# Optimization experiments

Measured on AMD Instinct MI355X. Metric: run time of the kernel, lower is better.

Reference implementation:

```python
import jax, jax.numpy as jnp
import numpy as np
import math

V, BLOCK, D, L, H, B, T = 32000, 1024, 1024, 6, 16, 4, 1024
HD = D // H
FF = 4 * D


def setup_inputs() -> dict:
    key = jax.random.key(0)
    ks = jax.random.split(key, 16)
    s = 0.02
    inp = {
        "idx": jax.random.randint(ks[0], (B, T), 0, V),
        "tok_emb": s * jax.random.normal(ks[1], (V, D), jnp.float32),
        "pos_emb": jnp.zeros((1, BLOCK, D), jnp.float32) + s * jax.random.normal(ks[2], (1, BLOCK, D), jnp.float32),
        "ln1_g": jnp.ones((L, D), jnp.float32),
        "ln1_b": jnp.zeros((L, D), jnp.float32),
        "qkv_w": s * jax.random.normal(ks[3], (L, 3 * D, D), jnp.float32),
        "proj_w": s * jax.random.normal(ks[4], (L, D, D), jnp.float32),
        "ln2_g": jnp.ones((L, D), jnp.float32),
        "ln2_b": jnp.zeros((L, D), jnp.float32),
        "mlp_w1": s * jax.random.normal(ks[5], (L, FF, D), jnp.float32),
        "mlp_b1": jnp.zeros((L, FF), jnp.float32),
        "mlp_w2": s * jax.random.normal(ks[6], (L, D, FF), jnp.float32),
        "mlp_b2": jnp.zeros((L, D), jnp.float32),
        "lnf_g": jnp.ones((D,), jnp.float32),
        "lnf_b": jnp.zeros((D,), jnp.float32),
        "head_w": s * jax.random.normal(ks[7], (V, D), jnp.float32),
    }
    return inp


def _layernorm(x, g, b, eps=1e-5):
    mu = jnp.mean(x, axis=-1, keepdims=True)
    var = jnp.mean(jnp.square(x - mu), axis=-1, keepdims=True)
    return (x - mu) * jax.lax.rsqrt(var + eps) * g + b


def _attn(x, qkv_w, proj_w):
    b, t, c = x.shape
    qkv = jnp.einsum('btc,fc->btf', x, qkv_w)  # [B,T,3D]
    q, k, v = jnp.split(qkv, 3, axis=-1)
    q = q.reshape(b, t, H, HD)
    k = k.reshape(b, t, H, HD)
    v = v.reshape(b, t, H, HD)
    att = jnp.einsum('bqhd,bkhd->bhqk', q, k) / math.sqrt(HD)
    causal = jnp.tril(jnp.ones((t, t), bool))
    att = jnp.where(causal[None, None], att, -jnp.inf)
    att = jax.nn.softmax(att, axis=-1)
    y = jnp.einsum('bhqk,bkhd->bqhd', att, v).reshape(b, t, c)
    return jnp.einsum('btc,fc->btf', y, proj_w)


def reference(idx, tok_emb, pos_emb, ln1_g, ln1_b, qkv_w, proj_w,
              ln2_g, ln2_b, mlp_w1, mlp_b1, mlp_w2, mlp_b2,
              lnf_g, lnf_b, head_w):
    t = idx.shape[1]
    x = tok_emb[idx] + pos_emb[:, :t, :]
    for i in range(L):
        h = _layernorm(x, ln1_g[i], ln1_b[i])
        x = x + _attn(h, qkv_w[i], proj_w[i])
        h = _layernorm(x, ln2_g[i], ln2_b[i])
        h = jax.nn.gelu(jnp.einsum('btc,fc->btf', h, mlp_w1[i]) + mlp_b1[i], approximate=False)
        x = x + jnp.einsum('btf,cf->btc', h, mlp_w2[i]) + mlp_b2[i]
    x = _layernorm(x, lnf_g, lnf_b)
    logits = jnp.einsum('btc,vc->btv', x, head_w)
    return logits
```

## Files before the change

kernel.cpp:

```cpp
#include <hip/hip_runtime.h>
#include <hip/hip_bf16.h>
#include <math.h>

#define BB 4
#define TT 1024
#define DD 1024
#define HH 16
#define HDIM 64
#define FFD 4096
#define VV 32000
#define LL 6
#define BT (BB * TT)

typedef __bf16 bf16;
typedef bf16 bf16x8 __attribute__((ext_vector_type(8)));
typedef bf16 bf16x4 __attribute__((ext_vector_type(4)));
typedef float f32x4 __attribute__((ext_vector_type(4)));

__device__ __forceinline__ void gload16(const void* g, void* l) {
    __builtin_amdgcn_global_load_lds((__attribute__((address_space(1))) unsigned int*)(g),
                                     (__attribute__((address_space(3))) unsigned int*)(l),
                                     16, 0, 0);
}

__global__ __launch_bounds__(256) void embed_k(const int* __restrict__ idx,
                                               const float* __restrict__ tok,
                                               const float* __restrict__ pos,
                                               float* __restrict__ x) {
    int row = blockIdx.x;
    int tid = threadIdx.x;
    int t = row & (TT - 1);
    int token = idx[row];
    float4 a = *(const float4*)(tok + (size_t)token * DD + tid * 4);
    float4 p = *(const float4*)(pos + (size_t)t * DD + tid * 4);
    *(float4*)(x + (size_t)row * DD + tid * 4) =
        make_float4(a.x + p.x, a.y + p.y, a.z + p.z, a.w + p.w);
}

__global__ __launch_bounds__(256) void cvt_bf16_k(const float* __restrict__ in,
                                                  bf16* __restrict__ out, long n) {
    long i0 = ((long)blockIdx.x * 256 + threadIdx.x) * 8;
    long stride = (long)gridDim.x * 256 * 8;
    for (long i = i0; i < n; i += stride) {
        float4 v0 = *(const float4*)(in + i);
        float4 v1 = *(const float4*)(in + i + 4);
        bf16x8 o;
        o[0] = (bf16)v0.x; o[1] = (bf16)v0.y; o[2] = (bf16)v0.z; o[3] = (bf16)v0.w;
        o[4] = (bf16)v1.x; o[5] = (bf16)v1.y; o[6] = (bf16)v1.z; o[7] = (bf16)v1.w;
        *(bf16x8*)(out + i) = o;
    }
}

__global__ __launch_bounds__(256) void layernorm_k(const float* __restrict__ in,
                                                   bf16* __restrict__ out,
                                                   const float* __restrict__ g,
                                                   const float* __restrict__ b) {
    __shared__ float red[256];
    int row = blockIdx.x;
    int tid = threadIdx.x;
    const float* ip = in + (size_t)row * DD;
    float4 v = *(const float4*)(ip + tid * 4);

    float s = v.x + v.y + v.z + v.w;
    red[tid] = s; __syncthreads();
    for (int st = 128; st > 0; st >>= 1) { if (tid < st) red[tid] += red[tid + st]; __syncthreads(); }
    float mu = red[0] * (1.0f / DD);
    __syncthreads();

    float d0 = v.x - mu, d1 = v.y - mu, d2 = v.z - mu, d3 = v.w - mu;
    red[tid] = d0 * d0 + d1 * d1 + d2 * d2 + d3 * d3; __syncthreads();
    for (int st = 128; st > 0; st >>= 1) { if (tid < st) red[tid] += red[tid + st]; __syncthreads(); }
    float var = red[0] * (1.0f / DD);
    float rs = rsqrtf(var + 1e-5f);

    float4 gv = *(const float4*)(g + tid * 4);
    float4 bv = *(const float4*)(b + tid * 4);
    bf16x4 o;
    o[0] = (bf16)(d0 * rs * gv.x + bv.x);
    o[1] = (bf16)(d1 * rs * gv.y + bv.y);
    o[2] = (bf16)(d2 * rs * gv.z + bv.z);
    o[3] = (bf16)(d3 * rs * gv.w + bv.w);
    *(bf16x4*)(out + (size_t)row * DD + tid * 4) = o;
}

template <bool BIAS, bool GELU, bool OBF>
__global__ __launch_bounds__(512, 2) void gemm_256(const bf16* __restrict__ A,
                                                   const bf16* __restrict__ W,
                                                   const float* __restrict__ bias,
                                                   void* __restrict__ Cv,
                                                   int M, int N, int K) {
    __shared__ char lds[2 * 65536];
    const int tid = threadIdx.x;
    const int lane = tid & 63, wave = tid >> 6;
    const int c = lane & 15, g = lane >> 4;

    const int nm = M >> 8;
    const int nwg = gridDim.x;
    const int wgid = (blockIdx.x & 7) * (nwg >> 3) + (blockIdx.x >> 3);
    const int m0 = (wgid % nm) * 256, n0 = (wgid / nm) * 256;
    const int wm = wave >> 2, wn = wave & 3;

    const int srow = tid >> 2;
    const int lq = (tid & 3) ^ ((tid >> 3) & 3);
    const bf16* Asrc = A + (size_t)(m0 + srow) * K + lq * 8;
    const bf16* Bsrc = W + (size_t)(n0 + srow) * K + lq * 8;
    const size_t K128 = (size_t)128 * K;

    const int key = (c >> 1) & 3;
    const int rdA = (wm * 128 + c) * 64 + ((g ^ key) * 16);
    const int rdB = 32768 + (wn * 64 + c) * 64 + ((g ^ key) * 16);

    f32x4 acc[8][4] = {};
    const int NT = K >> 6;
    const int NH = 4 * NT;

#define STAGEH(H)                                                             \
    if ((H) < NH) {                                                           \
        const int t2_ = (H) >> 2, h_ = (H) & 3;                               \
        const bf16* s_ = ((h_ & 1) ? Bsrc : Asrc) + (size_t)t2_ * 64 + (h_ >> 1) * 32; \
        char* d_ = lds + (t2_ & 1) * 65536 + (h_ & 1) * 32768 + (h_ >> 1) * 16384 + tid * 16; \
        gload16(s_, d_);                                                      \
        gload16(s_ + K128, d_ + 8192);                                        \
    }

#define MFMA16(base)                                                          \
    __builtin_amdgcn_s_setprio(1);                                            \
    _Pragma("unroll")                                                         \
    for (int fi = 0; fi < 4; ++fi) {                                          \
        _Pragma("unroll")                                                     \
        for (int fj = 0; fj < 4; ++fj)                                        \
            acc[(base) + fi][fj] = __builtin_amdgcn_mfma_f32_16x16x32_bf16(   \
                bA[fi], bB[fj], acc[(base) + fi][fj], 0, 0, 0);               \
    }                                                                         \
    __builtin_amdgcn_s_setprio(0);

    STAGEH(0); STAGEH(1); STAGEH(2); STAGEH(3); STAGEH(4);
    asm volatile("s_waitcnt vmcnt(6)" ::: "memory");
    __builtin_amdgcn_sched_barrier(0);
    __builtin_amdgcn_s_barrier();
    __builtin_amdgcn_sched_barrier(0);

    for (int kt = 0; kt < NT; ++kt) {
        const char* bp = lds + (kt & 1) * 65536;
        bf16x8 bA[4], bB[4];
#pragma unroll
        for (int fj = 0; fj < 4; ++fj) bB[fj] = *(const bf16x8*)(bp + rdB + fj * 1024);
#pragma unroll
        for (int fi = 0; fi < 4; ++fi) bA[fi] = *(const bf16x8*)(bp + rdA + fi * 1024);
        STAGEH(4 * kt + 5);
        asm volatile("s_waitcnt lgkmcnt(0)" ::: "memory");
        __builtin_amdgcn_sched_barrier(0);
        MFMA16(0)
#pragma unroll
        for (int fi = 0; fi < 4; ++fi) bA[fi] = *(const bf16x8*)(bp + rdA + (4 + fi) * 1024);
        STAGEH(4 * kt + 6);
        asm volatile("s_waitcnt lgkmcnt(0)" ::: "memory");
        __builtin_amdgcn_sched_barrier(0);
        MFMA16(4)
        if (kt + 1 < NT) { asm volatile("s_waitcnt vmcnt(6)" ::: "memory"); }
        else             { asm volatile("s_waitcnt vmcnt(0)" ::: "memory"); }
        __builtin_amdgcn_sched_barrier(0);
        __builtin_amdgcn_s_barrier();
        __builtin_amdgcn_sched_barrier(0);
#pragma unroll
        for (int fj = 0; fj < 4; ++fj) bB[fj] = *(const bf16x8*)(bp + rdB + 16384 + fj * 1024);
#pragma unroll
        for (int fi = 0; fi < 4; ++fi) bA[fi] = *(const bf16x8*)(bp + rdA + 16384 + fi * 1024);
        STAGEH(4 * kt + 7);
        asm volatile("s_waitcnt lgkmcnt(0)" ::: "memory");
        __builtin_amdgcn_sched_barrier(0);
        MFMA16(0)
#pragma unroll
        for (int fi = 0; fi < 4; ++fi) bA[fi] = *(const bf16x8*)(bp + rdA + 16384 + (4 + fi) * 1024);
        STAGEH(4 * kt + 8);
        asm volatile("s_waitcnt lgkmcnt(0)" ::: "memory");
        __builtin_amdgcn_sched_barrier(0);
        MFMA16(4)
        if (kt + 2 < NT)      { asm volatile("s_waitcnt vmcnt(6)" ::: "memory"); }
        else if (kt + 2 == NT){ asm volatile("s_waitcnt vmcnt(4)" ::: "memory"); }
        __builtin_amdgcn_sched_barrier(0);
        __builtin_amdgcn_s_barrier();
        __builtin_amdgcn_sched_barrier(0);
    }
#undef STAGEH
#undef MFMA16

    const int orow  = m0 + wm * 128 + g * 4;
    const int ocol0 = n0 + wn * 64 + c;
#pragma unroll
    for (int fj = 0; fj < 4; ++fj) {
        const int col = ocol0 + fj * 16;
        float bs = 0.f;
        if (BIAS) bs = bias[col];
#pragma unroll
        for (int fi = 0; fi < 8; ++fi) {
#pragma unroll
            for (int r = 0; r < 4; ++r) {
                int row = orow + fi * 16 + r;
                float v = acc[fi][fj][r] + bs;
                if (GELU) v = 0.5f * v * (1.0f + erff(v * 0.70710678118654752f));
                if (OBF) ((bf16*)Cv)[(size_t)row * N + col] = (bf16)v;
                else     __builtin_nontemporal_store(v, (float*)Cv + (size_t)row * N + col);
            }
        }
    }
}

template <bool ADD, bool BIAS>
__global__ __launch_bounds__(256, 2) void gemm_128p(const bf16* __restrict__ A,
                                                    const bf16* __restrict__ W,
                                                    const float* __restrict__ bias,
                                                    float* __restrict__ C,
                                                    int M, int N, int K) {
    __shared__ char lds[2 * 32768];
    const int tid = threadIdx.x;
    const int lane = tid & 63, wave = tid >> 6;
    const int c = lane & 15, g = lane >> 4;

    const int nm = M >> 7;
    const int nwg = gridDim.x;
    const int wgid = (blockIdx.x & 7) * (nwg >> 3) + (blockIdx.x >> 3);
    const int m0 = (wgid % nm) * 128, n0 = (wgid / nm) * 128;
    const int wm = wave >> 1, wn = wave & 1;

    const int srow = tid >> 2;
    const int lq = (tid & 3) ^ ((tid >> 3) & 3);
    const bf16* Asrc = A + (size_t)(m0 + srow) * K + lq * 8;
    const bf16* Bsrc = W + (size_t)(n0 + srow) * K + lq * 8;
    const size_t K64 = (size_t)64 * K;

    const int key = (c >> 1) & 3;
    const int rdA = (wm * 64 + c) * 64 + ((g ^ key) * 16);
    const int rdB = 16384 + (wn * 64 + c) * 64 + ((g ^ key) * 16);

    f32x4 acc[4][4] = {};
    const int NT = K >> 6;
    const int NH = 4 * NT;

#define STAGEH(H)                                                             \
    if ((H) < NH) {                                                           \
        const int t2_ = (H) >> 2, h_ = (H) & 3;                               \
        const bf16* s_ = ((h_ & 1) ? Bsrc : Asrc) + (size_t)t2_ * 64 + (h_ >> 1) * 32; \
        char* d_ = lds + (t2_ & 1) * 32768 + (h_ & 1) * 16384 + (h_ >> 1) * 8192 + tid * 16; \
        gload16(s_, d_);                                                      \
        gload16(s_ + K64, d_ + 4096);                                         \
    }

#define MFMA16()                                                              \
    __builtin_amdgcn_s_setprio(1);                                            \
    _Pragma("unroll")                                                         \
    for (int fi = 0; fi < 4; ++fi) {                                          \
        _Pragma("unroll")                                                     \
        for (int fj = 0; fj < 4; ++fj)                                       \
            acc[fi][fj] = __builtin_amdgcn_mfma_f32_16x16x32_bf16(            \
                bA[fi], bB[fj], acc[fi][fj], 0, 0, 0);                        \
    }                                                                         \
    __builtin_amdgcn_s_setprio(0);

    STAGEH(0); STAGEH(1); STAGEH(2); STAGEH(3); STAGEH(4); STAGEH(5);
    asm volatile("s_waitcnt vmcnt(8)" ::: "memory");
    __builtin_amdgcn_sched_barrier(0);
    __builtin_amdgcn_s_barrier();
    __builtin_amdgcn_sched_barrier(0);

    for (int kt = 0; kt < NT; ++kt) {
        const char* bp = lds + (kt & 1) * 32768;
        bf16x8 bA[4], bB[4];
#pragma unroll
        for (int fj = 0; fj < 4; ++fj) bB[fj] = *(const bf16x8*)(bp + rdB + fj * 1024);
#pragma unroll
        for (int fi = 0; fi < 4; ++fi) bA[fi] = *(const bf16x8*)(bp + rdA + fi * 1024);
        STAGEH(4 * kt + 6); STAGEH(4 * kt + 7);
        asm volatile("s_waitcnt lgkmcnt(0)" ::: "memory");
        __builtin_amdgcn_sched_barrier(0);
        MFMA16()
        if (kt + 1 < NT) { asm volatile("s_waitcnt vmcnt(8)" ::: "memory"); }
        else             { asm volatile("s_waitcnt vmcnt(0)" ::: "memory"); }
        __builtin_amdgcn_sched_barrier(0);
        __builtin_amdgcn_s_barrier();
        __builtin_amdgcn_sched_barrier(0);
#pragma unroll
        for (int fj = 0; fj < 4; ++fj) bB[fj] = *(const bf16x8*)(bp + rdB + 8192 + fj * 1024);
#pragma unroll
        for (int fi = 0; fi < 4; ++fi) bA[fi] = *(const bf16x8*)(bp + rdA + 8192 + fi * 1024);
        STAGEH(4 * kt + 8); STAGEH(4 * kt + 9);
        asm volatile("s_waitcnt lgkmcnt(0)" ::: "memory");
        __builtin_amdgcn_sched_barrier(0);
        MFMA16()
        if (kt + 2 < NT)       { asm volatile("s_waitcnt vmcnt(8)" ::: "memory"); }
        else if (kt + 2 == NT) { asm volatile("s_waitcnt vmcnt(4)" ::: "memory"); }
        __builtin_amdgcn_sched_barrier(0);
        __builtin_amdgcn_s_barrier();
        __builtin_amdgcn_sched_barrier(0);
    }
#undef STAGEH
#undef MFMA16

    const int orow  = m0 + wm * 64 + g * 4;
    const int ocol0 = n0 + wn * 64 + c;
#pragma unroll
    for (int fj = 0; fj < 4; ++fj) {
        const int col = ocol0 + fj * 16;
        float bs = 0.f;
        if (BIAS) bs = bias[col];
#pragma unroll
        for (int fi = 0; fi < 4; ++fi) {
#pragma unroll
            for (int r = 0; r < 4; ++r) {
                int row = orow + fi * 16 + r;
                float v = acc[fi][fj][r] + bs;
                float* p = C + (size_t)row * N + col;
                if (ADD) *p += v;
                else     __builtin_nontemporal_store(v, p);
            }
        }
    }
}

__global__ __launch_bounds__(256) void vprep_k(const bf16* __restrict__ qkv,
                                               bf16* __restrict__ Vt) {
    __shared__ bf16 Vls[64 * 72];
    const int tid = threadIdx.x;
    const int t0 = blockIdx.x * 64;
    const int h = blockIdx.y, b = blockIdx.z;
    const int row = tid >> 3, ch = tid & 7;

    const bf16* src = qkv + ((size_t)(b * TT + t0 + row)) * 3072 + 2048 + h * 64 + ch * 8;
    bf16x8 v0 = *(const bf16x8*)(src);
    bf16x8 v1 = *(const bf16x8*)(src + (size_t)32 * 3072);
#pragma unroll
    for (int j = 0; j < 8; ++j) {
        Vls[(ch * 8 + j) * 72 + row]      = v0[j];
        Vls[(ch * 8 + j) * 72 + row + 32] = v1[j];
    }
    __syncthreads();

    const int dr = tid >> 3;
    bf16* dst = Vt + ((size_t)((b * HH + h) * 64 + dr)) * 1024 + t0 + ch * 8;
    bf16x8 o0 = *(const bf16x8*)(Vls + dr * 72 + ch * 8);
    bf16x8 o1 = *(const bf16x8*)(Vls + (dr + 32) * 72 + ch * 8);
    *(bf16x8*)(dst) = o0;
    *(bf16x8*)(dst + (size_t)32 * 1024) = o1;
}

__global__ __launch_bounds__(512) void fattn_k(const bf16* __restrict__ qkv,
                                               const bf16* __restrict__ Vt,
                                               bf16* __restrict__ y) {
    __shared__ bf16 Ks[2][64 * 64];
    __shared__ bf16 Vs[2][64 * 64];
    __shared__ bf16 Ps[8][16 * 72];
    const int tid = threadIdx.x, lane = tid & 63, wave = tid >> 6;
    const int g = lane >> 4, c = lane & 15;
    const int q0 = (gridDim.x - 1 - blockIdx.x) * 128;
    const int h = blockIdx.y, b = blockIdx.z;
    const size_t qbase = (size_t)b * TT * 3072;

    const int qrow = q0 + wave * 16 + c;
    const bf16* qp = qkv + qbase + (size_t)qrow * 3072 + h * 64;
    bf16x8 qf0 = *(const bf16x8*)(qp + g * 8);
    bf16x8 qf1 = *(const bf16x8*)(qp + 32 + g * 8);

    const int srow = tid >> 3;
    const int lq = (tid & 7) ^ (srow & 7);
    const bf16* Ksrc = qkv + qbase + 1024 + h * 64 + (size_t)srow * 3072 + lq * 8;
    const bf16* Vsrc = Vt + ((size_t)(b * HH + h) * 64 + srow) * 1024 + lq * 8;

    float mO[4] = {-1e30f, -1e30f, -1e30f, -1e30f};
    float lO[4] = {0.f, 0.f, 0.f, 0.f};
    f32x4 acc[4] = {};

    bf16* pw = Ps[wave];
    const int ntiles = (q0 >> 6) + 2;
    const int qg0 = q0 + wave * 16 + 4 * g;
    const int cs = c & 7;

#define STAGE_KV(t_, buf_)                                                        \
    {                                                                             \
        const int kk_ = (t_) * 64;                                                \
        gload16(Ksrc + (size_t)kk_ * 3072, (char*)Ks[buf_] + tid * 16);           \
        gload16(Vsrc + kk_,                (char*)Vs[buf_] + tid * 16);           \
    }

    STAGE_KV(0, 0)

    for (int t = 0; t < ntiles; ++t) {
        const int k0 = t * 64;
        if (t + 1 < ntiles) {
            STAGE_KV(t + 1, (t + 1) & 1)
            asm volatile("s_waitcnt vmcnt(2)" ::: "memory");
        } else {
            asm volatile("s_waitcnt vmcnt(0)" ::: "memory");
        }
        __builtin_amdgcn_sched_barrier(0);
        __builtin_amdgcn_s_barrier();
        __builtin_amdgcn_sched_barrier(0);

        const bf16* kb = Ks[t & 1];
        const bf16* vb = Vs[t & 1];

        f32x4 s[4] = {};
#pragma unroll
        for (int j = 0; j < 4; ++j) {
            const bf16* kr = kb + (16 * j + c) * 64;
            bf16x8 kf0 = *(const bf16x8*)(kr + ((g ^ cs) * 8));
            bf16x8 kf1 = *(const bf16x8*)(kr + (((4 + g) ^ cs) * 8));
            s[j] = __builtin_amdgcn_mfma_f32_16x16x32_bf16(qf0, kf0, s[j], 0, 0, 0);
            s[j] = __builtin_amdgcn_mfma_f32_16x16x32_bf16(qf1, kf1, s[j], 0, 0, 0);
        }

        float mt_[4];
        bool need = false;
#pragma unroll
        for (int r = 0; r < 4; ++r) {
            const int qg = qg0 + r;
            float a0 = s[0][r] * 0.125f, a1 = s[1][r] * 0.125f;
            float a2 = s[2][r] * 0.125f, a3 = s[3][r] * 0.125f;
            if (k0 + c > qg)      a0 = -1e30f;
            if (k0 + 16 + c > qg) a1 = -1e30f;
            if (k0 + 32 + c > qg) a2 = -1e30f;
            if (k0 + 48 + c > qg) a3 = -1e30f;
            s[0][r] = a0; s[1][r] = a1; s[2][r] = a2; s[3][r] = a3;
            float mt = fmaxf(fmaxf(a0, a1), fmaxf(a2, a3));
            mt = fmaxf(mt, __shfl_xor(mt, 1));
            mt = fmaxf(mt, __shfl_xor(mt, 2));
            mt = fmaxf(mt, __shfl_xor(mt, 4));
            mt = fmaxf(mt, __shfl_xor(mt, 8));
            mt_[r] = mt;
            need |= (mt > mO[r]);
        }
        if (__any(need)) {
#pragma unroll
            for (int r = 0; r < 4; ++r) {
                float mn = fmaxf(mO[r], mt_[r]);
                float sc = __expf(mO[r] - mn);
                mO[r] = mn;
                lO[r] *= sc;
                acc[0][r] *= sc; acc[1][r] *= sc; acc[2][r] *= sc; acc[3][r] *= sc;
            }
        }
#pragma unroll
        for (int r = 0; r < 4; ++r) {
            float e0 = __expf(s[0][r] - mO[r]);
            float e1 = __expf(s[1][r] - mO[r]);
            float e2 = __expf(s[2][r] - mO[r]);
            float e3 = __expf(s[3][r] - mO[r]);
            lO[r] += (e0 + e1) + (e2 + e3);
            bf16* pr = pw + (4 * g + r) * 72;
            pr[c] = (bf16)e0; pr[16 + c] = (bf16)e1;
            pr[32 + c] = (bf16)e2; pr[48 + c] = (bf16)e3;
        }

#pragma unroll
        for (int ks = 0; ks < 2; ++ks) {
            bf16x8 pf = *(const bf16x8*)(pw + c * 72 + ks * 32 + g * 8);
#pragma unroll
            for (int jb = 0; jb < 4; ++jb) {
                const int d = 16 * jb + c;
                bf16x8 vf = *(const bf16x8*)(vb + d * 64 + (((ks * 4 + g) ^ cs) * 8));
                acc[jb] = __builtin_amdgcn_mfma_f32_16x16x32_bf16(pf, vf, acc[jb], 0, 0, 0);
            }
        }
        __builtin_amdgcn_s_barrier();
        __builtin_amdgcn_sched_barrier(0);
    }
#undef STAGE_KV

#pragma unroll
    for (int r = 0; r < 4; ++r) {
        float l = lO[r];
        l += __shfl_xor(l, 1);
        l += __shfl_xor(l, 2);
        l += __shfl_xor(l, 4);
        l += __shfl_xor(l, 8);
        float invl = 1.0f / l;
        size_t orow = (size_t)(b * TT + qg0 + r) * DD + h * 64;
#pragma unroll
        for (int jb = 0; jb < 4; ++jb)
            y[orow + jb * 16 + c] = (bf16)(acc[jb][r] * invl);
    }
}

extern "C" void kernel_launch(void* const* d_in, const int* in_sizes, int n_in,
                              void* d_out, int out_size, void* d_ws, size_t ws_size,
                              hipStream_t stream) {
    const int*   idx     = (const int*)d_in[0];
    const float* tok_emb = (const float*)d_in[1];
    const float* pos_emb = (const float*)d_in[2];
    const float* ln1_g   = (const float*)d_in[3];
    const float* ln1_b   = (const float*)d_in[4];
    const float* qkv_w   = (const float*)d_in[5];
    const float* proj_w  = (const float*)d_in[6];
    const float* ln2_g   = (const float*)d_in[7];
    const float* ln2_b   = (const float*)d_in[8];
    const float* mlp_w1  = (const float*)d_in[9];
    const float* mlp_b1  = (const float*)d_in[10];
    const float* mlp_w2  = (const float*)d_in[11];
    const float* mlp_b2  = (const float*)d_in[12];
    const float* lnf_g   = (const float*)d_in[13];
    const float* lnf_b   = (const float*)d_in[14];
    const float* head_w  = (const float*)d_in[15];
    float* out = (float*)d_out;

    char* ws = (char*)d_ws;
    float* x      = (float*)ws;
    bf16*  qkv_bf = (bf16*)(ws + (16ull << 20));
    bf16*  Vt     = (bf16*)(ws + (40ull << 20));
    bf16*  h_bf   = (bf16*)(ws + (48ull << 20));
    bf16*  y_bf   = (bf16*)(ws + (56ull << 20));
    bf16*  ff_bf  = (bf16*)(ws + (64ull << 20));
    bf16*  wbuf   = (bf16*)(ws + (96ull << 20));
    bf16*  hw_bf  = (bf16*)(ws + (56ull << 20));

    embed_k<<<BT, 256, 0, stream>>>(idx, tok_emb, pos_emb, x);

    for (int l = 0; l < LL; ++l) {
        layernorm_k<<<BT, 256, 0, stream>>>(x, h_bf, ln1_g + (size_t)l * DD, ln1_b + (size_t)l * DD);
        cvt_bf16_k<<<2048, 256, 0, stream>>>(qkv_w + (size_t)l * 3 * DD * DD, wbuf, (long)3 * DD * DD);
        gemm_256<false, false, true><<<(BT / 256) * (3 * DD / 256), 512, 0, stream>>>(
            h_bf, wbuf, nullptr, qkv_bf, BT, 3 * DD, DD);
        vprep_k<<<dim3(TT / 64, HH, BB), 256, 0, stream>>>(qkv_bf, Vt);
        fattn_k<<<dim3(TT / 128, HH, BB), 512, 0, stream>>>(qkv_bf, Vt, y_bf);
        cvt_bf16_k<<<2048, 256, 0, stream>>>(proj_w + (size_t)l * DD * DD, wbuf, (long)DD * DD);
        gemm_128p<true, false><<<(BT / 128) * (DD / 128), 256, 0, stream>>>(
            y_bf, wbuf, nullptr, x, BT, DD, DD);
        layernorm_k<<<BT, 256, 0, stream>>>(x, h_bf, ln2_g + (size_t)l * DD, ln2_b + (size_t)l * DD);
        cvt_bf16_k<<<2048, 256, 0, stream>>>(mlp_w1 + (size_t)l * FFD * DD, wbuf, (long)FFD * DD);
        gemm_256<true, true, true><<<(BT / 256) * (FFD / 256), 512, 0, stream>>>(
            h_bf, wbuf, mlp_b1 + (size_t)l * FFD, ff_bf, BT, FFD, DD);
        cvt_bf16_k<<<2048, 256, 0, stream>>>(mlp_w2 + (size_t)l * DD * FFD, wbuf, (long)DD * FFD);
        gemm_128p<true, true><<<(BT / 128) * (DD / 128), 256, 0, stream>>>(
            ff_bf, wbuf, mlp_b2 + (size_t)l * DD, x, BT, DD, FFD);
    }

    layernorm_k<<<BT, 256, 0, stream>>>(x, h_bf, lnf_g, lnf_b);
    cvt_bf16_k<<<4096, 256, 0, stream>>>(head_w, hw_bf, (long)VV * DD);
    gemm_256<false, false, false><<<(BT / 256) * (VV / 256), 512, 0, stream>>>(
        h_bf, hw_bf, nullptr, out, BT, VV, DD);
}
```

Before: 1.932 ms.

## Use exp2 softmax, skip masking on full tiles, pack P stores with permuted V layout

```diff
diff --git a/kernel.cpp b/kernel.cpp
--- a/kernel.cpp
+++ b/kernel.cpp
@@ -337,8 +337,13 @@
 
     const int dr = tid >> 3;
     bf16* dst = Vt + ((size_t)((b * HH + h) * 64 + dr)) * 1024 + t0 + ch * 8;
-    bf16x8 o0 = *(const bf16x8*)(Vls + dr * 72 + ch * 8);
-    bf16x8 o1 = *(const bf16x8*)(Vls + (dr + 32) * 72 + ch * 8);
+    bf16x8 o0, o1;
+#pragma unroll
+    for (int i = 0; i < 8; ++i) {
+        const int tt = 2 * ch + (i >> 2) + 16 * (i & 3);
+        o0[i] = Vls[dr * 72 + tt];
+        o1[i] = Vls[(dr + 32) * 72 + tt];
+    }
     *(bf16x8*)(dst) = o0;
     *(bf16x8*)(dst + (size_t)32 * 1024) = o1;
 }
@@ -354,6 +359,7 @@
     const int q0 = (gridDim.x - 1 - blockIdx.x) * 128;
     const int h = blockIdx.y, b = blockIdx.z;
     const size_t qbase = (size_t)b * TT * 3072;
+    const float SC = 0.125f * 1.4426950408889634f;
 
     const int qrow = q0 + wave * 16 + c;
     const bf16* qp = qkv + qbase + (size_t)qrow * 3072 + h * 64;
@@ -408,17 +414,20 @@
             s[j] = __builtin_amdgcn_mfma_f32_16x16x32_bf16(qf1, kf1, s[j], 0, 0, 0);
         }
 
+        const bool full = (t + 2 < ntiles);
         float mt_[4];
         bool need = false;
 #pragma unroll
         for (int r = 0; r < 4; ++r) {
             const int qg = qg0 + r;
-            float a0 = s[0][r] * 0.125f, a1 = s[1][r] * 0.125f;
-            float a2 = s[2][r] * 0.125f, a3 = s[3][r] * 0.125f;
-            if (k0 + c > qg)      a0 = -1e30f;
-            if (k0 + 16 + c > qg) a1 = -1e30f;
-            if (k0 + 32 + c > qg) a2 = -1e30f;
-            if (k0 + 48 + c > qg) a3 = -1e30f;
+            float a0 = s[0][r] * SC, a1 = s[1][r] * SC;
+            float a2 = s[2][r] * SC, a3 = s[3][r] * SC;
+            if (!full) {
+                if (k0 + c > qg)      a0 = -1e30f;
+                if (k0 + 16 + c > qg) a1 = -1e30f;
+                if (k0 + 32 + c > qg) a2 = -1e30f;
+                if (k0 + 48 + c > qg) a3 = -1e30f;
+            }
             s[0][r] = a0; s[1][r] = a1; s[2][r] = a2; s[3][r] = a3;
             float mt = fmaxf(fmaxf(a0, a1), fmaxf(a2, a3));
             mt = fmaxf(mt, __shfl_xor(mt, 1));
@@ -432,7 +441,7 @@
 #pragma unroll
             for (int r = 0; r < 4; ++r) {
                 float mn = fmaxf(mO[r], mt_[r]);
-                float sc = __expf(mO[r] - mn);
+                float sc = exp2f(mO[r] - mn);
                 mO[r] = mn;
                 lO[r] *= sc;
                 acc[0][r] *= sc; acc[1][r] *= sc; acc[2][r] *= sc; acc[3][r] *= sc;
@@ -440,14 +449,14 @@
         }
 #pragma unroll
         for (int r = 0; r < 4; ++r) {
-            float e0 = __expf(s[0][r] - mO[r]);
-            float e1 = __expf(s[1][r] - mO[r]);
-            float e2 = __expf(s[2][r] - mO[r]);
-            float e3 = __expf(s[3][r] - mO[r]);
+            float e0 = exp2f(s[0][r] - mO[r]);
+            float e1 = exp2f(s[1][r] - mO[r]);
+            float e2 = exp2f(s[2][r] - mO[r]);
+            float e3 = exp2f(s[3][r] - mO[r]);
             lO[r] += (e0 + e1) + (e2 + e3);
-            bf16* pr = pw + (4 * g + r) * 72;
-            pr[c] = (bf16)e0; pr[16 + c] = (bf16)e1;
-            pr[32 + c] = (bf16)e2; pr[48 + c] = (bf16)e3;
+            bf16x4 pk;
+            pk[0] = (bf16)e0; pk[1] = (bf16)e1; pk[2] = (bf16)e2; pk[3] = (bf16)e3;
+            *(bf16x4*)(pw + (4 * g + r) * 72 + c * 4) = pk;
         }
 
 #pragma unroll
```

Result: slower. 1.974 ms (+2.2%).
